# Performance work log

Hardware: AMD Instinct MI355X
Metric: run time of the kernel (lower is better)

Reference implementation:

```python
import jax, jax.numpy as jnp
import numpy as np

N_NODES = 8192
N_EDGES = 524288
N_PAIRS = 262144
N_TYPES = 86


def _gcn_conv(x, W, b, src, dst, n):
    # PyG GCNConv: transform, add self-loops, symmetric degree normalization,
    # scatter-add aggregation at destination nodes.
    xw = x @ W  # [N, F_out]
    loop = jnp.arange(n, dtype=src.dtype)
    s = jnp.concatenate([src, loop])
    d = jnp.concatenate([dst, loop])
    deg = jax.ops.segment_sum(jnp.ones(d.shape, xw.dtype), d, num_segments=n)
    dinv = jnp.where(deg > 0, jax.lax.rsqrt(deg), 0.0)  # deg^{-1/2}, 0 for isolated
    coef = dinv[s] * dinv[d]  # [E+N]
    out = jax.ops.segment_sum(xw[s] * coef[:, None], d, num_segments=n)
    return out + b


def setup_inputs() -> dict:
    key = jax.random.key(0)
    ks = jax.random.split(key, 10)
    x = jax.random.normal(ks[0], (N_NODES, N_NODES), dtype=jnp.float32)
    edge_index = jax.random.randint(ks[1], (2, N_EDGES), 0, N_NODES, dtype=jnp.int32)
    drug1_idx = jax.random.randint(ks[2], (N_PAIRS,), 0, N_NODES, dtype=jnp.int32)
    drug2_idx = jax.random.randint(ks[3], (N_PAIRS,), 0, N_NODES, dtype=jnp.int32)
    W1 = jax.random.normal(ks[4], (N_NODES, 128), dtype=jnp.float32) / np.sqrt(N_NODES)
    b1 = jnp.zeros((128,), jnp.float32)
    W2 = jax.random.normal(ks[5], (128, 64), dtype=jnp.float32) / np.sqrt(128.0)
    b2 = jnp.zeros((64,), jnp.float32)
    Wfc = jax.random.normal(ks[6], (128, N_TYPES), dtype=jnp.float32) / np.sqrt(128.0)
    bfc = jnp.zeros((N_TYPES,), jnp.float32)
    return {"x": x, "edge_index": edge_index, "drug1_idx": drug1_idx,
            "drug2_idx": drug2_idx, "W1": W1, "b1": b1, "W2": W2, "b2": b2,
            "Wfc": Wfc, "bfc": bfc}


def reference(x, edge_index, drug1_idx, drug2_idx, W1, b1, W2, b2, Wfc, bfc):
    n = x.shape[0]
    src, dst = edge_index[0], edge_index[1]
    h = jax.nn.relu(_gcn_conv(x, W1, b1, src, dst, n))
    # dropout p=0.3 is identity at inference (training=False)
    h = jax.nn.relu(_gcn_conv(h, W2, b2, src, dst, n))
    combined = jnp.concatenate([h[drug1_idx], h[drug2_idx]], axis=1)  # [P, 128]
    return jax.nn.sigmoid(combined @ Wfc + bfc)
```

## Files before the change

### kernel.cpp

```cpp
#include <hip/hip_runtime.h>
#include <math.h>
#include <stdint.h>
#include <stddef.h>

#define N_NODES 8192
#define N_EDGES 524288
#define N_PAIRS 262144
#define N_TYPES 86
#define F1 128
#define F2 64

typedef unsigned short ushort_t;
typedef unsigned int uint_t;
typedef __attribute__((ext_vector_type(8))) short bfrag;
typedef __attribute__((ext_vector_type(4))) float ffrag;

typedef __attribute__((address_space(3))) char lds_char;
typedef __attribute__((address_space(1))) const char g_char;

__device__ __forceinline__ void gload16(const void* g, void* l) {
  __builtin_amdgcn_global_load_lds((const g_char*)g, (lds_char*)l, 16, 0, 0);
}

__device__ inline ushort_t f2bf(float f) {
  uint_t u = __float_as_uint(f);
  uint_t r = u + 0x7fffu + ((u >> 16) & 1u);
  return (ushort_t)(r >> 16);
}
__device__ inline float bf2f(ushort_t h) {
  return __uint_as_float(((uint_t)h) << 16);
}


__global__ void zero_k(int* __restrict__ p) {
  p[blockIdx.x * 256 + threadIdx.x] = 0;
}

__global__ void count_deg_k(const int* __restrict__ dst, int* __restrict__ cnt) {
  int e = blockIdx.x * blockDim.x + threadIdx.x;
  if (e < N_EDGES) atomicAdd(&cnt[dst[e]], 1);
}

__global__ void scan_k(const int* __restrict__ cnt, int* __restrict__ rp,
                       int* __restrict__ fill, float* __restrict__ dinv) {
  __shared__ int s[1024];
  int t = threadIdx.x;
  int v[8];
  int sum = 0;
#pragma unroll
  for (int i = 0; i < 8; i++) {
    v[i] = cnt[t * 8 + i];
    dinv[t * 8 + i] = 1.0f / sqrtf((float)(v[i] + 1));
    sum += v[i];
  }
  s[t] = sum;
  __syncthreads();
  for (int off = 1; off < 1024; off <<= 1) {
    int add = (t >= off) ? s[t - off] : 0;
    __syncthreads();
    s[t] += add;
    __syncthreads();
  }
  int excl = s[t] - sum;
#pragma unroll
  for (int i = 0; i < 8; i++) {
    rp[t * 8 + i] = excl;
    fill[t * 8 + i] = excl;
    excl += v[i];
  }
  if (t == 1023) rp[N_NODES] = excl;
}

__global__ void scatter_k(const int* __restrict__ src, const int* __restrict__ dst,
                          int* fill, int* __restrict__ csr) {
  int e = blockIdx.x * blockDim.x + threadIdx.x;
  if (e < N_EDGES) {
    int d = dst[e];
    int pos = atomicAdd(&fill[d], 1);
    csr[pos] = src[e];
  }
}


__global__ __launch_bounds__(256) void w1split_k(const float* __restrict__ W1,
                                                 ushort_t* __restrict__ W1th,
                                                 ushort_t* __restrict__ W1tl) {
  __shared__ ushort_t lh[32 * 65];
  __shared__ ushort_t ll[32 * 65];
  int tid = threadIdx.x;
  int k0 = blockIdx.x * 64;
  int n0 = blockIdx.y * 32;
#pragma unroll
  for (int i = 0; i < 8; i++) {
    int c = tid + 256 * i;
    int kr = c >> 5, nc = c & 31;
    float v = W1[(size_t)(k0 + kr) * F1 + n0 + nc];
    ushort_t h = f2bf(v);
    ushort_t l = f2bf(v - bf2f(h));
    lh[nc * 65 + kr] = h;
    ll[nc * 65 + kr] = l;
  }
  __syncthreads();
#pragma unroll
  for (int i = 0; i < 2; i++) {
    int c = tid + 256 * i;
    int buf = c >> 8;
    int cc = c & 255;
    int nr = cc >> 3, kc = cc & 7;
    const ushort_t* l = buf ? ll : lh;
    uint4 u;
    u.x = (uint_t)l[nr * 65 + kc * 8 + 0] | ((uint_t)l[nr * 65 + kc * 8 + 1] << 16);
    u.y = (uint_t)l[nr * 65 + kc * 8 + 2] | ((uint_t)l[nr * 65 + kc * 8 + 3] << 16);
    u.z = (uint_t)l[nr * 65 + kc * 8 + 4] | ((uint_t)l[nr * 65 + kc * 8 + 5] << 16);
    u.w = (uint_t)l[nr * 65 + kc * 8 + 6] | ((uint_t)l[nr * 65 + kc * 8 + 7] << 16);
    ushort_t* dst = (buf ? W1tl : W1th) + (size_t)(n0 + nr) * N_NODES + k0 + kc * 8;
    *(uint4*)dst = u;
  }
}


#define OAH 0
#define OAL 4096
#define OBB(b) (8192 + (b) * 16384)

#define SCHED0 __builtin_amdgcn_sched_barrier(0)
#define WAITVM(N)  do { asm volatile("s_waitcnt vmcnt(" #N ")" ::: "memory"); SCHED0; } while (0)
#define WAITVML(N) do { asm volatile("s_waitcnt vmcnt(" #N ") lgkmcnt(0)" ::: "memory"); SCHED0; } while (0)

__global__ __launch_bounds__(256, 4) void gemm1_mfma_k(const float* __restrict__ x,
                                                       const ushort_t* __restrict__ W1th,
                                                       const ushort_t* __restrict__ W1tl,
                                                       float* __restrict__ part, int kspan) {
  __shared__ __align__(16) char lds[40960];
  int tid = threadIdx.x;
  int wave = tid >> 6, lane = tid & 63;
  int wr = wave >> 1, wc = wave & 1;
  int lrow = lane & 15, kgrp = lane >> 4;
  int m_blk = blockIdx.y * 64;
  int kbase = blockIdx.x * kspan;
  int ktiles = kspan >> 5;

  int s0 = (5 * blockIdx.y + 4 * blockIdx.x) & (ktiles - 1);

  int bq = wave;
  int b_row = bq * 32 + (lane >> 2);
  int b_kel = ((lane & 3) ^ ((lane >> 2) & 3)) << 3;

  ffrag acc[2][4];
#pragma unroll
  for (int mi = 0; mi < 2; mi++)
#pragma unroll
    for (int ni = 0; ni < 4; ni++) acc[mi][ni] = (ffrag)(0.0f);

  float4 av[2];

#define LOADA(K0)                                                                    \
  {                                                                                  \
    _Pragma("unroll") for (int i = 0; i < 2; i++) {                                  \
      int c = tid + 256 * i;                                                         \
      int row = c >> 3, c4 = c & 7;                                                  \
      av[i] = *(const float4*)&x[(size_t)(m_blk + row) * N_NODES + (K0) + 4 * c4];   \
    }                                                                                \
  }

#define ISSUE_B(K0, BSEL)                                                            \
  {                                                                                  \
    _Pragma("unroll") for (int i = 0; i < 2; i++) {                                  \
      const ushort_t* gh = W1th + (size_t)(b_row + i * 16) * N_NODES + (K0) + b_kel; \
      gload16(gh, lds + OBB(BSEL) + bq * 2048 + i * 1024);                           \
      const ushort_t* gl = W1tl + (size_t)(b_row + i * 16) * N_NODES + (K0) + b_kel; \
      gload16(gl, lds + OBB(BSEL) + 8192 + bq * 2048 + i * 1024);                    \
    }                                                                                \
  }

#define STOREA()                                                                     \
  {                                                                                  \
    _Pragma("unroll") for (int i = 0; i < 2; i++) {                                  \
      int c = tid + 256 * i;                                                         \
      int row = c >> 3, c4 = c & 7;                                                  \
      float f0 = av[i].x, f1 = av[i].y, f2 = av[i].z, f3 = av[i].w;                  \
      ushort_t h0 = f2bf(f0), h1 = f2bf(f1), h2 = f2bf(f2), h3 = f2bf(f3);           \
      ushort_t l0 = f2bf(f0 - bf2f(h0)), l1 = f2bf(f1 - bf2f(h1));                   \
      ushort_t l2 = f2bf(f2 - bf2f(h2)), l3 = f2bf(f3 - bf2f(h3));                   \
      uint2 hp, lp;                                                                  \
      hp.x = (uint_t)h0 | ((uint_t)h1 << 16); hp.y = (uint_t)h2 | ((uint_t)h3 << 16);\
      lp.x = (uint_t)l0 | ((uint_t)l1 << 16); lp.y = (uint_t)l2 | ((uint_t)l3 << 16);\
      uint_t off = row * 64 + ((c4 * 8) ^ ((row & 3) << 4));                         \
      *(uint2*)(lds + OAH + off) = hp;                                               \
      *(uint2*)(lds + OAL + off) = lp;                                               \
    }                                                                                \
  }

#define COMPUTE(BSEL)                                                                \
  {                                                                                  \
    bfrag bh[4], bl[4];                                                              \
    _Pragma("unroll") for (int ni = 0; ni < 4; ni++) {                               \
      int brow = wc * 64 + ni * 16 + lrow;                                           \
      uint_t boff = brow * 64 + ((kgrp * 16) ^ ((brow & 3) << 4));                   \
      bh[ni] = *(const bfrag*)(lds + OBB(BSEL) + boff);                              \
      bl[ni] = *(const bfrag*)(lds + OBB(BSEL) + 8192 + boff);                       \
    }                                                                                \
    _Pragma("unroll") for (int mi = 0; mi < 2; mi++) {                               \
      int arow = wr * 32 + mi * 16 + lrow;                                           \
      uint_t aoff = arow * 64 + ((kgrp * 16) ^ ((arow & 3) << 4));                   \
      bfrag ah = *(const bfrag*)(lds + OAH + aoff);                                  \
      bfrag al = *(const bfrag*)(lds + OAL + aoff);                                  \
      _Pragma("unroll") for (int ni = 0; ni < 4; ni++) {                             \
        acc[mi][ni] = __builtin_amdgcn_mfma_f32_16x16x32_bf16(ah, bh[ni], acc[mi][ni], 0, 0, 0); \
        acc[mi][ni] = __builtin_amdgcn_mfma_f32_16x16x32_bf16(ah, bl[ni], acc[mi][ni], 0, 0, 0); \
        acc[mi][ni] = __builtin_amdgcn_mfma_f32_16x16x32_bf16(al, bh[ni], acc[mi][ni], 0, 0, 0); \
      }                                                                              \
    }                                                                                \
  }

  LOADA(kbase + (s0 << 5));
  ISSUE_B(kbase + (s0 << 5), 0);
  WAITVM(4);
  STOREA();
  WAITVML(0);
  __builtin_amdgcn_s_barrier();
  SCHED0;

  int sp = s0;
  for (int s = 0; s < ktiles; ++s) {
    int more = (s + 1 < ktiles);
    int spn = sp + 1; if (spn == ktiles) spn = 0;
    if (more) {
      int k0n = kbase + (spn << 5);
      LOADA(k0n);
      SCHED0;
      ISSUE_B(k0n, (s + 1) & 1);
      SCHED0;
    }
    __builtin_amdgcn_s_setprio(1);
    COMPUTE(s & 1);
    __builtin_amdgcn_s_setprio(0);
    __builtin_amdgcn_s_barrier();
    SCHED0;
    if (more) {
      WAITVM(4);
      STOREA();
      WAITVML(0);
      __builtin_amdgcn_s_barrier();
      SCHED0;
    }
    sp = spn;
  }

  float* outp = part + (size_t)blockIdx.x * (N_NODES * F1);
#pragma unroll
  for (int mi = 0; mi < 2; mi++) {
#pragma unroll
    for (int ni = 0; ni < 4; ni++) {
      int col = wc * 64 + ni * 16 + lrow;
#pragma unroll
      for (int r = 0; r < 4; r++) {
        int row = m_blk + wr * 32 + mi * 16 + kgrp * 4 + r;
        outp[(size_t)row * F1 + col] = acc[mi][ni][r];
      }
    }
  }
#undef LOADA
#undef ISSUE_B
#undef STOREA
#undef COMPUTE
}

__global__ void reduceS_k(const float* __restrict__ part, float* __restrict__ xw1, int S) {
  int i = blockIdx.x * blockDim.x + threadIdx.x;
  float4 a = ((const float4*)part)[i];
  for (int s = 1; s < S; s++) {
    float4 b = ((const float4*)(part + (size_t)s * N_NODES * F1))[i];
    a.x += b.x; a.y += b.y; a.z += b.z; a.w += b.w;
  }
  ((float4*)xw1)[i] = a;
}


template <int F>
__global__ void agg_k(const float* __restrict__ xw, const int* __restrict__ csr,
                      const int* __restrict__ rp, const float* __restrict__ dinv,
                      const float* __restrict__ bias, float* __restrict__ hout) {
  int node = blockIdx.x;
  int f = threadIdx.x;
  __shared__ int sidx[F];
  __shared__ float sdv[F];
  int beg = rp[node], end = rp[node + 1];
  float acc = 0.f;
  for (int base = beg; base < end; base += F) {
    int n = end - base;
    if (n > F) n = F;
    __syncthreads();
    if (f < n) {
      int s = csr[base + f];
      sidx[f] = s;
      sdv[f] = dinv[s];
    }
    __syncthreads();
    for (int i = 0; i < n; i++) acc += xw[(size_t)sidx[i] * F + f] * sdv[i];
  }
  float dv = dinv[node];
  float v = (acc + xw[(size_t)node * F + f] * dv) * dv + bias[f];
  hout[(size_t)node * F + f] = v > 0.f ? v : 0.f;
}


__global__ __launch_bounds__(256) void gemm2_k(const float* __restrict__ h1,
                                               const float* __restrict__ W2,
                                               float* __restrict__ xw2) {
  __shared__ float W2s[F1 * F2];
  __shared__ float As[16 * F1];
  int tid = threadIdx.x;
  int r0 = blockIdx.x * 16;
#pragma unroll
  for (int j = 0; j < 8; j++)
    ((float4*)W2s)[tid + 256 * j] = ((const float4*)W2)[tid + 256 * j];
#pragma unroll
  for (int j = 0; j < 2; j++)
    ((float4*)As)[tid + 256 * j] = ((const float4*)(h1 + (size_t)r0 * F1))[tid + 256 * j];
  __syncthreads();
  int r = tid >> 4, c4 = tid & 15;
  float4 acc = make_float4(0.f, 0.f, 0.f, 0.f);
#pragma unroll 8
  for (int k = 0; k < F1; k++) {
    float a = As[r * F1 + k];
    float4 bv = *(float4*)&W2s[k * F2 + 4 * c4];
    acc.x += a * bv.x; acc.y += a * bv.y; acc.z += a * bv.z; acc.w += a * bv.w;
  }
  *(float4*)&xw2[(size_t)(r0 + r) * F2 + 4 * c4] = acc;
}


__global__ void pboth_k(const float* __restrict__ h2, const float* __restrict__ Wfc,
                        float* __restrict__ P) {
  __shared__ float hs[64 * 16];
  int tid = threadIdx.x;
  int r0 = blockIdx.x * 16;
  for (int idx = tid; idx < 256; idx += 192) {
    int row = idx >> 4, k4 = idx & 15;
    float4 h = *(const float4*)&h2[(size_t)(r0 + row) * F2 + 4 * k4];
    hs[(4 * k4 + 0) * 16 + row] = h.x;
    hs[(4 * k4 + 1) * 16 + row] = h.y;
    hs[(4 * k4 + 2) * 16 + row] = h.z;
    hs[(4 * k4 + 3) * 16 + row] = h.w;
  }
  __syncthreads();
  if (tid < 172) {
    int half = tid < 86 ? 0 : 1;
    int j = tid - 86 * half;
    const float* wp = Wfc + (size_t)(64 * half) * N_TYPES + j;
    float acc[16];
#pragma unroll
    for (int r = 0; r < 16; r++) acc[r] = 0.f;
    for (int k = 0; k < 64; k++) {
      float w = wp[(size_t)k * N_TYPES];
      const float* hk = &hs[k * 16];
#pragma unroll
      for (int r = 0; r < 16; r++) acc[r] += hk[r] * w;
    }
#pragma unroll
    for (int r = 0; r < 16; r++) P[(size_t)(r0 + r) * 172 + tid] = acc[r];
  }
}


__global__ void final_k(const float* __restrict__ P, const int* __restrict__ d1,
                        const int* __restrict__ d2, const float* __restrict__ bfc,
                        float* __restrict__ out) {
  int gid = blockIdx.x * blockDim.x + threadIdx.x;
  if (gid >= N_PAIRS * 43) return;
  int p = gid / 43;
  int j = gid - p * 43;
  int a = d1[p], b = d2[p];
  float2 v1 = *(const float2*)&P[(size_t)a * 172 + 2 * j];
  float2 v2 = *(const float2*)&P[(size_t)b * 172 + 86 + 2 * j];
  float2 bb = *(const float2*)&bfc[2 * j];
  float z0 = v1.x + v2.x + bb.x;
  float z1 = v1.y + v2.y + bb.y;
  float2 o;
  o.x = 1.0f / (1.0f + expf(-z0));
  o.y = 1.0f / (1.0f + expf(-z1));
  *(float2*)&out[(size_t)p * 86 + 2 * j] = o;
}


extern "C" void kernel_launch(void* const* d_in, const int* in_sizes, int n_in,
                              void* d_out, int out_size, void* d_ws, size_t ws_size,
                              hipStream_t stream) {
  const float* x   = (const float*)d_in[0];
  const int*   ei  = (const int*)d_in[1];
  const int*   d1  = (const int*)d_in[2];
  const int*   d2  = (const int*)d_in[3];
  const float* W1  = (const float*)d_in[4];
  const float* b1  = (const float*)d_in[5];
  const float* W2  = (const float*)d_in[6];
  const float* b2  = (const float*)d_in[7];
  const float* Wfc = (const float*)d_in[8];
  const float* bfc = (const float*)d_in[9];
  float* out = (float*)d_out;

  const int* esrc = ei;
  const int* edst = ei + N_EDGES;

  char* w = (char*)d_ws;
  size_t off = 0;
  auto alloc = [&](size_t bytes) -> char* {
    char* p = w + off;
    off += (bytes + 255) & ~(size_t)255;
    return p;
  };
  int*      cnt  = (int*)alloc((size_t)N_NODES * 4);
  float*    dinv = (float*)alloc((size_t)N_NODES * 4);
  int*      rp   = (int*)alloc((size_t)(N_NODES + 1) * 4);
  int*      fill = (int*)alloc((size_t)N_NODES * 4);
  int*      csr  = (int*)alloc((size_t)N_EDGES * 4);
  ushort_t* W1th = (ushort_t*)alloc((size_t)N_NODES * F1 * 2);
  ushort_t* W1tl = (ushort_t*)alloc((size_t)N_NODES * F1 * 2);
  float*    h1   = (float*)alloc((size_t)N_NODES * F1 * 4);
  float*    xw2  = (float*)alloc((size_t)N_NODES * F2 * 4);
  float*    h2   = (float*)alloc((size_t)N_NODES * F2 * 4);
  float*    P    = (float*)alloc((size_t)N_NODES * 172 * 4);

  size_t partBytes = (size_t)N_NODES * F1 * 4;
  int S = 8;
  while (S > 1 && off + (size_t)S * partBytes > ws_size) S >>= 1;
  float* part = (float*)alloc((size_t)S * partBytes);
  float* xw1 = part;
  if (off > ws_size) return;

  zero_k<<<N_NODES / 256, 256, 0, stream>>>(cnt);
  count_deg_k<<<N_EDGES / 256, 256, 0, stream>>>(edst, cnt);
  scan_k<<<1, 1024, 0, stream>>>(cnt, rp, fill, dinv);
  scatter_k<<<N_EDGES / 256, 256, 0, stream>>>(esrc, edst, fill, csr);

  w1split_k<<<dim3(N_NODES / 64, F1 / 32), 256, 0, stream>>>(W1, W1th, W1tl);
  gemm1_mfma_k<<<dim3(S, N_NODES / 64), 256, 0, stream>>>(x, W1th, W1tl, part, N_NODES / S);
  if (S > 1)
    reduceS_k<<<(N_NODES * F1 / 4) / 256, 256, 0, stream>>>(part, xw1, S);
  agg_k<F1><<<N_NODES, F1, 0, stream>>>(xw1, csr, rp, dinv, b1, h1);

  gemm2_k<<<N_NODES / 16, 256, 0, stream>>>(h1, W2, xw2);
  agg_k<F2><<<N_NODES, F2, 0, stream>>>(xw2, csr, rp, dinv, b2, h2);

  pboth_k<<<N_NODES / 16, 192, 0, stream>>>(h2, Wfc, P);
  final_k<<<(N_PAIRS * 43 + 255) / 256, 256, 0, stream>>>(P, d1, d2, bfc, out);
}
```

Measured before the change: 265.4 us.

## Drop low-part of W1 split and double GEMM1 M-tile to 128 rows

```diff
diff --git a/kernel.cpp b/kernel.cpp
--- a/kernel.cpp
+++ b/kernel.cpp
@@ -82,11 +82,9 @@
 }
 
 
-__global__ __launch_bounds__(256) void w1split_k(const float* __restrict__ W1,
-                                                 ushort_t* __restrict__ W1th,
-                                                 ushort_t* __restrict__ W1tl) {
+__global__ __launch_bounds__(256) void w1t_k(const float* __restrict__ W1,
+                                             ushort_t* __restrict__ W1t) {
   __shared__ ushort_t lh[32 * 65];
-  __shared__ ushort_t ll[32 * 65];
   int tid = threadIdx.x;
   int k0 = blockIdx.x * 64;
   int n0 = blockIdx.y * 32;
@@ -94,120 +92,117 @@
   for (int i = 0; i < 8; i++) {
     int c = tid + 256 * i;
     int kr = c >> 5, nc = c & 31;
-    float v = W1[(size_t)(k0 + kr) * F1 + n0 + nc];
-    ushort_t h = f2bf(v);
-    ushort_t l = f2bf(v - bf2f(h));
-    lh[nc * 65 + kr] = h;
-    ll[nc * 65 + kr] = l;
+    lh[nc * 65 + kr] = f2bf(W1[(size_t)(k0 + kr) * F1 + n0 + nc]);
   }
   __syncthreads();
-#pragma unroll
-  for (int i = 0; i < 2; i++) {
-    int c = tid + 256 * i;
-    int buf = c >> 8;
-    int cc = c & 255;
-    int nr = cc >> 3, kc = cc & 7;
-    const ushort_t* l = buf ? ll : lh;
+  {
+    int c = tid;
+    int nr = c >> 3, kc = c & 7;
     uint4 u;
-    u.x = (uint_t)l[nr * 65 + kc * 8 + 0] | ((uint_t)l[nr * 65 + kc * 8 + 1] << 16);
-    u.y = (uint_t)l[nr * 65 + kc * 8 + 2] | ((uint_t)l[nr * 65 + kc * 8 + 3] << 16);
-    u.z = (uint_t)l[nr * 65 + kc * 8 + 4] | ((uint_t)l[nr * 65 + kc * 8 + 5] << 16);
-    u.w = (uint_t)l[nr * 65 + kc * 8 + 6] | ((uint_t)l[nr * 65 + kc * 8 + 7] << 16);
-    ushort_t* dst = (buf ? W1tl : W1th) + (size_t)(n0 + nr) * N_NODES + k0 + kc * 8;
-    *(uint4*)dst = u;
-  }
-}
-
-
-#define OAH 0
-#define OAL 4096
-#define OBB(b) (8192 + (b) * 16384)
+    u.x = (uint_t)lh[nr * 65 + kc * 8 + 0] | ((uint_t)lh[nr * 65 + kc * 8 + 1] << 16);
+    u.y = (uint_t)lh[nr * 65 + kc * 8 + 2] | ((uint_t)lh[nr * 65 + kc * 8 + 3] << 16);
+    u.z = (uint_t)lh[nr * 65 + kc * 8 + 4] | ((uint_t)lh[nr * 65 + kc * 8 + 5] << 16);
+    u.w = (uint_t)lh[nr * 65 + kc * 8 + 6] | ((uint_t)lh[nr * 65 + kc * 8 + 7] << 16);
+    *(uint4*)(W1t + (size_t)(n0 + nr) * N_NODES + k0 + kc * 8) = u;
+  }
+}
+
+
+#define ALDS 0
+#define BLDS(b) (16384 + (b) * 8192)
 
 #define SCHED0 __builtin_amdgcn_sched_barrier(0)
 #define WAITVM(N)  do { asm volatile("s_waitcnt vmcnt(" #N ")" ::: "memory"); SCHED0; } while (0)
 #define WAITVML(N) do { asm volatile("s_waitcnt vmcnt(" #N ") lgkmcnt(0)" ::: "memory"); SCHED0; } while (0)
 
-__global__ __launch_bounds__(256, 4) void gemm1_mfma_k(const float* __restrict__ x,
-                                                       const ushort_t* __restrict__ W1th,
-                                                       const ushort_t* __restrict__ W1tl,
+__global__ __launch_bounds__(256, 2) void gemm1_mfma_k(const float* __restrict__ x,
+                                                       const ushort_t* __restrict__ W1t,
                                                        float* __restrict__ part, int kspan) {
-  __shared__ __align__(16) char lds[40960];
+  __shared__ __align__(16) char lds[32768];
   int tid = threadIdx.x;
   int wave = tid >> 6, lane = tid & 63;
   int wr = wave >> 1, wc = wave & 1;
   int lrow = lane & 15, kgrp = lane >> 4;
-  int m_blk = blockIdx.y * 64;
+  int m_blk = blockIdx.y * 128;
   int kbase = blockIdx.x * kspan;
   int ktiles = kspan >> 5;
-
-  int s0 = (5 * blockIdx.y + 4 * blockIdx.x) & (ktiles - 1);
+  int s0 = (5 * blockIdx.y + 3 * blockIdx.x) & (ktiles - 1);
+
+  int ar = tid >> 1, aq = tid & 1;
+  const float* abase = x + (size_t)(m_blk + ar) * N_NODES + aq * 16;
 
   int bq = wave;
   int b_row = bq * 32 + (lane >> 2);
   int b_kel = ((lane & 3) ^ ((lane >> 2) & 3)) << 3;
 
-  ffrag acc[2][4];
-#pragma unroll
-  for (int mi = 0; mi < 2; mi++)
+  ffrag acc[4][4];
+#pragma unroll
+  for (int mi = 0; mi < 4; mi++)
 #pragma unroll
     for (int ni = 0; ni < 4; ni++) acc[mi][ni] = (ffrag)(0.0f);
 
-  float4 av[2];
+  float4 av[4];
 
 #define LOADA(K0)                                                                    \
   {                                                                                  \
-    _Pragma("unroll") for (int i = 0; i < 2; i++) {                                  \
-      int c = tid + 256 * i;                                                         \
-      int row = c >> 3, c4 = c & 7;                                                  \
-      av[i] = *(const float4*)&x[(size_t)(m_blk + row) * N_NODES + (K0) + 4 * c4];   \
-    }                                                                                \
+    const float* p_ = abase + (K0);                                                  \
+    av[0] = *(const float4*)(p_ + 0);                                                \
+    av[1] = *(const float4*)(p_ + 4);                                                \
+    av[2] = *(const float4*)(p_ + 8);                                                \
+    av[3] = *(const float4*)(p_ + 12);                                               \
   }
 
 #define ISSUE_B(K0, BSEL)                                                            \
   {                                                                                  \
     _Pragma("unroll") for (int i = 0; i < 2; i++) {                                  \
-      const ushort_t* gh = W1th + (size_t)(b_row + i * 16) * N_NODES + (K0) + b_kel; \
-      gload16(gh, lds + OBB(BSEL) + bq * 2048 + i * 1024);                           \
-      const ushort_t* gl = W1tl + (size_t)(b_row + i * 16) * N_NODES + (K0) + b_kel; \
-      gload16(gl, lds + OBB(BSEL) + 8192 + bq * 2048 + i * 1024);                    \
+      const ushort_t* gp = W1t + (size_t)(b_row + i * 16) * N_NODES + (K0) + b_kel;  \
+      gload16(gp, lds + BLDS(BSEL) + bq * 2048 + i * 1024);                          \
     }                                                                                \
   }
 
 #define STOREA()                                                                     \
   {                                                                                  \
-    _Pragma("unroll") for (int i = 0; i < 2; i++) {                                  \
-      int c = tid + 256 * i;                                                         \
-      int row = c >> 3, c4 = c & 7;                                                  \
-      float f0 = av[i].x, f1 = av[i].y, f2 = av[i].z, f3 = av[i].w;                  \
-      ushort_t h0 = f2bf(f0), h1 = f2bf(f1), h2 = f2bf(f2), h3 = f2bf(f3);           \
-      ushort_t l0 = f2bf(f0 - bf2f(h0)), l1 = f2bf(f1 - bf2f(h1));                   \
-      ushort_t l2 = f2bf(f2 - bf2f(h2)), l3 = f2bf(f3 - bf2f(h3));                   \
-      uint2 hp, lp;                                                                  \
-      hp.x = (uint_t)h0 | ((uint_t)h1 << 16); hp.y = (uint_t)h2 | ((uint_t)h3 << 16);\
-      lp.x = (uint_t)l0 | ((uint_t)l1 << 16); lp.y = (uint_t)l2 | ((uint_t)l3 << 16);\
-      uint_t off = row * 64 + ((c4 * 8) ^ ((row & 3) << 4));                         \
-      *(uint2*)(lds + OAH + off) = hp;                                               \
-      *(uint2*)(lds + OAL + off) = lp;                                               \
+    float f[16];                                                                     \
+    f[0]=av[0].x; f[1]=av[0].y; f[2]=av[0].z; f[3]=av[0].w;                          \
+    f[4]=av[1].x; f[5]=av[1].y; f[6]=av[1].z; f[7]=av[1].w;                          \
+    f[8]=av[2].x; f[9]=av[2].y; f[10]=av[2].z; f[11]=av[2].w;                        \
+    f[12]=av[3].x; f[13]=av[3].y; f[14]=av[3].z; f[15]=av[3].w;                      \
+    ushort_t h[16], l[16];                                                           \
+    _Pragma("unroll") for (int j = 0; j < 16; j++) {                                 \
+      h[j] = f2bf(f[j]);                                                             \
+      l[j] = f2bf(f[j] - bf2f(h[j]));                                                \
     }                                                                                \
+    uint4 H0, H1, L0, L1;                                                            \
+    H0.x=(uint_t)h[0]|((uint_t)h[1]<<16);  H0.y=(uint_t)h[2]|((uint_t)h[3]<<16);     \
+    H0.z=(uint_t)h[4]|((uint_t)h[5]<<16);  H0.w=(uint_t)h[6]|((uint_t)h[7]<<16);     \
+    H1.x=(uint_t)h[8]|((uint_t)h[9]<<16);  H1.y=(uint_t)h[10]|((uint_t)h[11]<<16);   \
+    H1.z=(uint_t)h[12]|((uint_t)h[13]<<16); H1.w=(uint_t)h[14]|((uint_t)h[15]<<16);  \
+    L0.x=(uint_t)l[0]|((uint_t)l[1]<<16);  L0.y=(uint_t)l[2]|((uint_t)l[3]<<16);     \
+    L0.z=(uint_t)l[4]|((uint_t)l[5]<<16);  L0.w=(uint_t)l[6]|((uint_t)l[7]<<16);     \
+    L1.x=(uint_t)l[8]|((uint_t)l[9]<<16);  L1.y=(uint_t)l[10]|((uint_t)l[11]<<16);   \
+    L1.z=(uint_t)l[12]|((uint_t)l[13]<<16); L1.w=(uint_t)l[14]|((uint_t)l[15]<<16);  \
+    uint_t rb = ar * 128, rx = ar & 7;                                               \
+    *(uint4*)(lds + ALDS + rb + (((2*aq)   ^ rx) << 4)) = H0;                        \
+    *(uint4*)(lds + ALDS + rb + (((2*aq+1) ^ rx) << 4)) = H1;                        \
+    *(uint4*)(lds + ALDS + rb + (((4+2*aq) ^ rx) << 4)) = L0;                        \
+    *(uint4*)(lds + ALDS + rb + (((5+2*aq) ^ rx) << 4)) = L1;                        \
   }
 
 #define COMPUTE(BSEL)                                                                \
   {                                                                                  \
-    bfrag bh[4], bl[4];                                                              \
+    bfrag bh[4];                                                                     \
     _Pragma("unroll") for (int ni = 0; ni < 4; ni++) {                               \
       int brow = wc * 64 + ni * 16 + lrow;                                           \
-      uint_t boff = brow * 64 + ((kgrp * 16) ^ ((brow & 3) << 4));                   \
-      bh[ni] = *(const bfrag*)(lds + OBB(BSEL) + boff);                              \
-      bl[ni] = *(const bfrag*)(lds + OBB(BSEL) + 8192 + boff);                       \
+      uint_t boff = brow * 64 + ((kgrp ^ (brow & 3)) << 4);                          \
+      bh[ni] = *(const bfrag*)(lds + BLDS(BSEL) + boff);                             \
     }                                                                                \
-    _Pragma("unroll") for (int mi = 0; mi < 2; mi++) {                               \
-      int arow = wr * 32 + mi * 16 + lrow;                                           \
-      uint_t aoff = arow * 64 + ((kgrp * 16) ^ ((arow & 3) << 4));                   \
-      bfrag ah = *(const bfrag*)(lds + OAH + aoff);                                  \
-      bfrag al = *(const bfrag*)(lds + OAL + aoff);                                  \
+    _Pragma("unroll") for (int mi = 0; mi < 4; mi++) {                               \
+      int arow = wr * 64 + mi * 16 + lrow;                                           \
+      uint_t rb = arow * 128, rx = arow & 7;                                         \
+      bfrag ah = *(const bfrag*)(lds + ALDS + rb + ((kgrp ^ rx) << 4));              \
+      bfrag al = *(const bfrag*)(lds + ALDS + rb + (((4 + kgrp) ^ rx) << 4));        \
       _Pragma("unroll") for (int ni = 0; ni < 4; ni++) {                             \
         acc[mi][ni] = __builtin_amdgcn_mfma_f32_16x16x32_bf16(ah, bh[ni], acc[mi][ni], 0, 0, 0); \
-        acc[mi][ni] = __builtin_amdgcn_mfma_f32_16x16x32_bf16(ah, bl[ni], acc[mi][ni], 0, 0, 0); \
         acc[mi][ni] = __builtin_amdgcn_mfma_f32_16x16x32_bf16(al, bh[ni], acc[mi][ni], 0, 0, 0); \
       }                                                                              \
     }                                                                                \
@@ -215,7 +210,7 @@
 
   LOADA(kbase + (s0 << 5));
   ISSUE_B(kbase + (s0 << 5), 0);
-  WAITVM(4);
+  WAITVM(2);
   STOREA();
   WAITVML(0);
   __builtin_amdgcn_s_barrier();
@@ -238,7 +233,7 @@
     __builtin_amdgcn_s_barrier();
     SCHED0;
     if (more) {
-      WAITVM(4);
+      WAITVM(2);
       STOREA();
       WAITVML(0);
       __builtin_amdgcn_s_barrier();
@@ -249,13 +244,13 @@
 
   float* outp = part + (size_t)blockIdx.x * (N_NODES * F1);
 #pragma unroll
-  for (int mi = 0; mi < 2; mi++) {
+  for (int mi = 0; mi < 4; mi++) {
 #pragma unroll
     for (int ni = 0; ni < 4; ni++) {
       int col = wc * 64 + ni * 16 + lrow;
 #pragma unroll
       for (int r = 0; r < 4; r++) {
-        int row = m_blk + wr * 32 + mi * 16 + kgrp * 4 + r;
+        int row = m_blk + wr * 64 + mi * 16 + kgrp * 4 + r;
         outp[(size_t)row * F1 + col] = acc[mi][ni][r];
       }
     }
@@ -414,8 +409,7 @@
   int*      rp   = (int*)alloc((size_t)(N_NODES + 1) * 4);
   int*      fill = (int*)alloc((size_t)N_NODES * 4);
   int*      csr  = (int*)alloc((size_t)N_EDGES * 4);
-  ushort_t* W1th = (ushort_t*)alloc((size_t)N_NODES * F1 * 2);
-  ushort_t* W1tl = (ushort_t*)alloc((size_t)N_NODES * F1 * 2);
+  ushort_t* W1t  = (ushort_t*)alloc((size_t)N_NODES * F1 * 2);
   float*    h1   = (float*)alloc((size_t)N_NODES * F1 * 4);
   float*    xw2  = (float*)alloc((size_t)N_NODES * F2 * 4);
   float*    h2   = (float*)alloc((size_t)N_NODES * F2 * 4);
@@ -433,8 +427,8 @@
   scan_k<<<1, 1024, 0, stream>>>(cnt, rp, fill, dinv);
   scatter_k<<<N_EDGES / 256, 256, 0, stream>>>(esrc, edst, fill, csr);
 
-  w1split_k<<<dim3(N_NODES / 64, F1 / 32), 256, 0, stream>>>(W1, W1th, W1tl);
-  gemm1_mfma_k<<<dim3(S, N_NODES / 64), 256, 0, stream>>>(x, W1th, W1tl, part, N_NODES / S);
+  w1t_k<<<dim3(N_NODES / 64, F1 / 32), 256, 0, stream>>>(W1, W1t);
+  gemm1_mfma_k<<<dim3(S, N_NODES / 128), 256, 0, stream>>>(x, W1t, part, N_NODES / S);
   if (S > 1)
     reduceS_k<<<(N_NODES * F1 / 4) / 256, 256, 0, stream>>>(part, xw1, S);
   agg_k<F1><<<N_NODES, F1, 0, stream>>>(xw1, csr, rp, dinv, b1, h1);
```

After: 251.5 us (median of 2 runs). -5.2%, faster.
